# Optimization experiments

Hardware: AMD Instinct MI355X
Metric: run time of the kernel (lower is better)

The kernel has to match this reference:

```python
import jax, jax.numpy as jnp
import numpy as np

NUM_HEADS = 16


def _rope(x, c, s):
    # x: [T, H, D]; c, s: [T, D/2] -> rotate-half RoPE over full head_dim
    d2 = c.shape[-1]
    x1, x2 = x[..., :d2], x[..., d2:]
    c = c[:, None, :]
    s = s[:, None, :]
    return jnp.concatenate([x1 * c - x2 * s, x2 * c + x1 * s], axis=-1)


def setup_inputs() -> dict:
    key = jax.random.key(0)
    ks = jax.random.split(key, 4)
    B, L, dim = 8, 1024, 1024
    T = B * L
    D = dim // NUM_HEADS
    hidden_states = jax.random.normal(ks[0], (T, dim), dtype=jnp.float32)
    w_qkv = jax.random.normal(ks[1], (dim, 3 * dim), dtype=jnp.float32) * (dim ** -0.5)
    b_qkv = jnp.zeros((3 * dim,), dtype=jnp.float32)
    w_proj = jax.random.normal(ks[2], (dim, dim), dtype=jnp.float32) * (dim ** -0.5)
    b_proj = jnp.zeros((dim,), dtype=jnp.float32)
    # RoPE tables: positions restart at 0 for each packed sequence
    pos = jnp.tile(jnp.arange(L, dtype=jnp.float32), B)  # [T]
    inv_freq = 1.0 / (10000.0 ** (jnp.arange(0, D, 2, dtype=jnp.float32) / D))  # [D/2]
    freqs = pos[:, None] * inv_freq[None, :]  # [T, D/2]
    emb = jnp.concatenate([freqs, freqs], axis=-1)  # [T, D]
    cos = jnp.cos(emb)
    sin = jnp.sin(emb)
    cu_seqlens = (jnp.arange(B + 1, dtype=jnp.int32) * L)
    return {"hidden_states": hidden_states, "cos": cos, "sin": sin,
            "w_qkv": w_qkv, "b_qkv": b_qkv, "w_proj": w_proj, "b_proj": b_proj,
            "cu_seqlens": cu_seqlens}


def reference(hidden_states, cos, sin, w_qkv, b_qkv, w_proj, b_proj, cu_seqlens):
    T, dim = hidden_states.shape
    H = NUM_HEADS
    D = dim // H
    B = cu_seqlens.shape[0] - 1  # equal-length packed sequences
    L = T // B

    qkv = hidden_states @ w_qkv + b_qkv            # [T, 3*dim]
    qkv = qkv.reshape(T, 3, H, D)
    q, k, v = qkv[:, 0], qkv[:, 1], qkv[:, 2]       # [T, H, D]

    # module chunks cos/sin in half along last dim before apply_rotary_emb
    c = cos[..., : D // 2].astype(jnp.float32)
    s = sin[..., : D // 2].astype(jnp.float32)
    q = _rope(q.astype(jnp.float32), c, s).astype(hidden_states.dtype)
    k = _rope(k.astype(jnp.float32), c, s).astype(hidden_states.dtype)

    # varlen flash attention == block-diagonal attention; equal lengths -> reshape
    qb = q.reshape(B, L, H, D)
    kb = k.reshape(B, L, H, D)
    vb = v.reshape(B, L, H, D)
    scale = D ** -0.5
    scores = jnp.einsum("bqhd,bkhd->bhqk", qb, kb) * scale  # [B, H, L, L]
    probs = jax.nn.softmax(scores, axis=-1)
    out = jnp.einsum("bhqk,bkhd->bqhd", probs, vb)           # [B, L, H, D]
    out = out.reshape(T, dim)
    return out @ w_proj + b_proj
```

## Files before the change

kernel.cpp:

```cpp
#include <hip/hip_runtime.h>

typedef unsigned short ushort_t;
typedef __attribute__((ext_vector_type(8))) short short8;
typedef __attribute__((ext_vector_type(4))) float f32x4;

#define AS1 __attribute__((address_space(1)))
#define AS3 __attribute__((address_space(3)))

__device__ __forceinline__ ushort_t f2bf(float f) {
  unsigned int u = __builtin_bit_cast(unsigned int, f);
  u += 0x7fffu + ((u >> 16) & 1u);
  return (ushort_t)(u >> 16);
}

__device__ __forceinline__ unsigned int pack_bf2(float a, float b) {
  unsigned int ua = __builtin_bit_cast(unsigned int, a) + 0x8000u;
  unsigned int ub = __builtin_bit_cast(unsigned int, b) + 0x8000u;
  return (ua >> 16) | (ub & 0xffff0000u);
}

#if defined(__has_builtin)
#if __has_builtin(__builtin_amdgcn_cvt_pk_bf16_f32)
#define HAVE_CVT_PK_BF16 1
#endif
#if __has_builtin(__builtin_amdgcn_exp2f)
#define HAVE_EXP2 1
#endif
#endif

__device__ __forceinline__ unsigned int pack2(float a, float b) {
#ifdef HAVE_CVT_PK_BF16
  typedef __attribute__((ext_vector_type(2))) __bf16 bf2_t;
  bf2_t r = __builtin_amdgcn_cvt_pk_bf16_f32(a, b);
  return __builtin_bit_cast(unsigned int, r);
#else
  return pack_bf2(a, b);
#endif
}

__device__ __forceinline__ float fast_exp2(float x) {
#ifdef HAVE_EXP2
  return __builtin_amdgcn_exp2f(x);
#else
  return exp2f(x);
#endif
}

__device__ __forceinline__ void load_lds16(const ushort_t* g, ushort_t* l) {
  __builtin_amdgcn_global_load_lds((AS1 void*)g, (AS3 void*)l, 16, 0, 0);
}

#define MFMA16(a, b, c) __builtin_amdgcn_mfma_f32_16x16x32_bf16((a), (b), (c), 0, 0, 0)

__global__ __launch_bounds__(256) void k_prep(const float* __restrict__ hs,
                                              ushort_t* __restrict__ hsb,
                                              const float* __restrict__ wqkv,
                                              ushort_t* __restrict__ wqkvT,
                                              const float* __restrict__ wproj,
                                              ushort_t* __restrict__ wprojT) {
  __shared__ ushort_t t[64 * 65];
  const int bid = blockIdx.x;
  if (bid < 4096) {
    int i = bid * 256 + threadIdx.x;
    const float4* s4 = (const float4*)hs;
    float4 a = s4[(size_t)i * 2], b = s4[(size_t)i * 2 + 1];
    short8 o;
    o[0] = (short)f2bf(a.x); o[1] = (short)f2bf(a.y);
    o[2] = (short)f2bf(a.z); o[3] = (short)f2bf(a.w);
    o[4] = (short)f2bf(b.x); o[5] = (short)f2bf(b.y);
    o[6] = (short)f2bf(b.z); o[7] = (short)f2bf(b.w);
    *(short8*)(hsb + (size_t)i * 8) = o;
    return;
  }
  const float* src;
  ushort_t* dst;
  int C, bx, by;
  if (bid < 4864) { int idx = bid - 4096; src = wqkv; dst = wqkvT; C = 3072;
                    bx = idx % 48; by = idx / 48; }
  else            { int idx = bid - 4864; src = wproj; dst = wprojT; C = 1024;
                    bx = idx & 15; by = idx >> 4; }
  const int R = 1024;
  const int x0 = bx * 64, y0 = by * 64;
  const int c = threadIdx.x & 63, r0 = threadIdx.x >> 6;
#pragma unroll
  for (int i = 0; i < 16; ++i) {
    int r = r0 + i * 4;
    t[c * 65 + r] = f2bf(src[(size_t)(y0 + r) * C + x0 + c]);
  }
  __syncthreads();
#pragma unroll
  for (int i = 0; i < 16; ++i) {
    int rr = r0 + i * 4;
    dst[(size_t)(x0 + rr) * R + y0 + c] = t[rr * 65 + c];
  }
}

__global__ __launch_bounds__(512) void k_qkv_gemm_rope(
    const ushort_t* __restrict__ A, const ushort_t* __restrict__ Bt,
    const float* __restrict__ bias, const float* __restrict__ cosb,
    const float* __restrict__ sinb, ushort_t* __restrict__ Qb,
    ushort_t* __restrict__ Kb, ushort_t* __restrict__ Vp) {
  constexpr int K = 1024;
  __shared__ __align__(16) ushort_t As[256 * 64];
  __shared__ __align__(16) ushort_t Bs[128 * 64];
  const int tid = threadIdx.x, lane = tid & 63, wave = tid >> 6;
  const int quad = lane >> 4, ml = lane & 15;
  const int wm = wave & 3, wn = wave >> 2;
  const int L = blockIdx.x, xcd = L & 7, j = L >> 3;
  const int by = xcd * 4 + j / 24, bx = j % 24;
  const int m0 = by * 256, n0 = bx * 128;
  f32x4 acc[4][4] = {};

  for (int kt = 0; kt < K / 64; ++kt) {
    __syncthreads();
    {
      const int kk0 = kt * 64;
#pragma unroll
      for (int i = 0; i < 4; ++i) {
        int cch = i * 512 + tid;
        int r = cch >> 3, s = cch & 7, gs = s ^ (r & 7);
        load_lds16(A + (size_t)(m0 + r) * K + kk0 + gs * 8, As + cch * 8);
      }
#pragma unroll
      for (int i = 0; i < 2; ++i) {
        int cch = i * 512 + tid;
        int r = cch >> 3, s = cch & 7, gs = s ^ (r & 7);
        load_lds16(Bt + (size_t)(n0 + r) * K + kk0 + gs * 8, Bs + cch * 8);
      }
    }
    __syncthreads();
#pragma unroll
    for (int ks = 0; ks < 2; ++ks) {
      short8 af[4], bfr[4];
#pragma unroll
      for (int mb = 0; mb < 4; ++mb) {
        int row = wm * 64 + mb * 16 + ml;
        int gs = (ks * 4 + quad) ^ (row & 7);
        af[mb] = *(const short8*)(As + row * 64 + gs * 8);
      }
#pragma unroll
      for (int nb = 0; nb < 4; ++nb) {
        int row = wn * 64 + nb * 16 + ml;
        int gs = (ks * 4 + quad) ^ (row & 7);
        bfr[nb] = *(const short8*)(Bs + row * 64 + gs * 8);
      }
#pragma unroll
      for (int mb = 0; mb < 4; ++mb)
#pragma unroll
        for (int nb = 0; nb < 4; ++nb)
          acc[mb][nb] = MFMA16(af[mb], bfr[nb], acc[mb][nb]);
    }
  }

  const int ncol0 = n0 + wn * 64;
  const int sec = ncol0 >> 10;
  const int h = (ncol0 & 1023) >> 6;
  if (sec < 2) {
    ushort_t* dst = (sec == 0) ? Qb : Kb;
    const float qs = (sec == 0) ? 0.18033688011112042f : 1.0f;
#pragma unroll
    for (int mb = 0; mb < 4; ++mb) {
#pragma unroll
      for (int rg = 0; rg < 4; ++rg) {
        const int m = m0 + wm * 64 + mb * 16 + quad * 4 + rg;
        const int b = m >> 10, l = m & 1023;
        const size_t ob = ((size_t)(b * 16 + h) * 1024 + l) * 64;
#pragma unroll
        for (int nb = 0; nb < 2; ++nb) {
          const int d = nb * 16 + ml;
          float x1 = acc[mb][nb][rg] + bias[ncol0 + d];
          float x2 = acc[mb][nb + 2][rg] + bias[ncol0 + d + 32];
          float cv = cosb[(size_t)m * 64 + d] * qs;
          float sv = sinb[(size_t)m * 64 + d] * qs;
          dst[ob + d] = f2bf(x1 * cv - x2 * sv);
          dst[ob + d + 32] = f2bf(x2 * cv + x1 * sv);
        }
      }
    }
  } else {
    const int mrow = m0 + wm * 64;
    const int b = mrow >> 10, lB = mrow & 1023;
    ushort_t* vb = Vp + ((size_t)(b * 16 + h)) * 65536 + lB;
#pragma unroll
    for (int rg = 0; rg < 4; ++rg) {
#pragma unroll
      for (int nb = 0; nb < 4; ++nb) {
        const int d = nb * 16 + ml;
        const float bs = bias[ncol0 + d];
        uint2 w;
        w.x = pack_bf2(acc[0][nb][rg] + bs, acc[1][nb][rg] + bs);
        w.y = pack_bf2(acc[2][nb][rg] + bs, acc[3][nb][rg] + bs);
        *(uint2*)(vb + (size_t)d * 1024 + 16 * quad + 4 * rg) = w;
      }
    }
  }
}

__global__ __launch_bounds__(256, 4) void k_attn(const ushort_t* __restrict__ Qb,
                                                 const ushort_t* __restrict__ Kb,
                                                 const ushort_t* __restrict__ Vp,
                                                 ushort_t* __restrict__ Ob) {
  __shared__ __align__(16) ushort_t QP[8192];
  __shared__ __align__(16) ushort_t Ks[2][64 * 64];
  __shared__ __align__(16) ushort_t Vts[64 * 64];
  const int tid = threadIdx.x, lane = tid & 63, wave = tid >> 6;
  const int quad = lane >> 4, ml = lane & 15;
  const int bh = blockIdx.x & 127, qt = blockIdx.x >> 7;
  const int q0 = qt * 128;
  const size_t base = (size_t)bh * 65536;

#pragma unroll
  for (int i = 0; i < 4; ++i) {
    int cch = i * 256 + tid;
    int r = cch >> 3, s = cch & 7, gs = s ^ (r & 7);
    load_lds16(Qb + base + (size_t)(q0 + r) * 64 + gs * 8, QP + cch * 8);
  }
  __syncthreads();

  short8 qf[2][2];
#pragma unroll
  for (int mb = 0; mb < 2; ++mb)
#pragma unroll
    for (int ks = 0; ks < 2; ++ks) {
      int row = wave * 32 + mb * 16 + ml;
      int gs = (ks * 4 + quad) ^ (row & 7);
      qf[mb][ks] = *(const short8*)(QP + row * 64 + gs * 8);
    }

  ushort_t* Pw = QP + wave * 2048;

  const ushort_t* kg[2];
  const ushort_t* vg[2];
  ushort_t *kl[2], *vl[2];
#pragma unroll
  for (int i = 0; i < 2; ++i) {
    int cch = i * 256 + tid;
    int r = cch >> 3, gs = (cch & 7) ^ (r & 7);
    kg[i] = Kb + base + (size_t)r * 64 + gs * 8;
    kl[i] = Ks[0] + cch * 8;
    vg[i] = Vp + base + (size_t)r * 1024 + gs * 8;
    vl[i] = Vts + cch * 8;
  }
  const ushort_t* kfp[4][2];
  const ushort_t* vfp[4][2];
#pragma unroll
  for (int nb = 0; nb < 4; ++nb)
#pragma unroll
    for (int ks = 0; ks < 2; ++ks) {
      int row = nb * 16 + ml;
      int gs = (ks * 4 + quad) ^ (row & 7);
      kfp[nb][ks] = Ks[0] + row * 64 + gs * 8;
      vfp[nb][ks] = Vts + row * 64 + gs * 8;
    }
  const ushort_t* pfp[2][2];
#pragma unroll
  for (int mb = 0; mb < 2; ++mb)
#pragma unroll
    for (int ks = 0; ks < 2; ++ks) {
      int row = mb * 16 + ml;
      int gs = ((ks * 4 + quad) ^ row) & 7;
      pfp[mb][ks] = Pw + row * 64 + gs * 8;
    }
  ushort_t* pwp[2][4];
#pragma unroll
  for (int mb = 0; mb < 2; ++mb)
#pragma unroll
    for (int rg = 0; rg < 4; ++rg) {
      int row = mb * 16 + quad * 4 + rg;
      int g = ((ml >> 1) ^ row) & 7;
      pwp[mb][rg] = Pw + row * 64 + g * 8 + (ml & 1) * 4;
    }

  f32x4 Oacc[2][4] = {};
  float lsum[2][4] = {};

#pragma unroll
  for (int i = 0; i < 2; ++i) { load_lds16(kg[i], kl[i]); kg[i] += 4096; }
  __syncthreads();

#define ATTN_STEP(CUR, LAST)                                                  \
  {                                                                           \
    _Pragma("unroll") for (int i = 0; i < 2; ++i) {                           \
      load_lds16(vg[i], vl[i]);                                               \
      vg[i] += 64;                                                            \
      if (!(LAST)) {                                                          \
        load_lds16(kg[i], kl[i] + ((CUR) ^ 1) * 4096);                        \
        kg[i] += 4096;                                                        \
      }                                                                       \
    }                                                                         \
    f32x4 Sacc[2][4] = {};                                                    \
    __builtin_amdgcn_s_setprio(1);                                            \
    _Pragma("unroll") for (int nb = 0; nb < 4; ++nb)                          \
      _Pragma("unroll") for (int ks = 0; ks < 2; ++ks) {                      \
        short8 kf = *(const short8*)(kfp[nb][ks] + (CUR) * 4096);             \
        Sacc[0][nb] = MFMA16(qf[0][ks], kf, Sacc[0][nb]);                     \
        Sacc[1][nb] = MFMA16(qf[1][ks], kf, Sacc[1][nb]);                     \
      }                                                                       \
    __builtin_amdgcn_s_setprio(0);                                            \
    _Pragma("unroll") for (int mb = 0; mb < 2; ++mb) {                        \
      _Pragma("unroll") for (int rg = 0; rg < 4; ++rg) {                      \
        float p0 = fast_exp2(Sacc[mb][0][rg]);                                \
        float p1 = fast_exp2(Sacc[mb][1][rg]);                                \
        float p2 = fast_exp2(Sacc[mb][2][rg]);                                \
        float p3 = fast_exp2(Sacc[mb][3][rg]);                                \
        lsum[mb][rg] += (p0 + p1) + (p2 + p3);                                \
        uint2 w;                                                              \
        w.x = pack2(p0, p1);                                                  \
        w.y = pack2(p2, p3);                                                  \
        *(uint2*)pwp[mb][rg] = w;                                             \
      }                                                                       \
    }                                                                         \
    __syncthreads();                                                          \
    __builtin_amdgcn_s_setprio(1);                                            \
    _Pragma("unroll") for (int ks = 0; ks < 2; ++ks) {                        \
      short8 pf0 = *(const short8*)pfp[0][ks];                                \
      short8 pf1 = *(const short8*)pfp[1][ks];                                \
      _Pragma("unroll") for (int nb = 0; nb < 4; ++nb) {                      \
        short8 vf = *(const short8*)vfp[nb][ks];                              \
        Oacc[0][nb] = MFMA16(pf0, vf, Oacc[0][nb]);                           \
        Oacc[1][nb] = MFMA16(pf1, vf, Oacc[1][nb]);                           \
      }                                                                       \
    }                                                                         \
    __builtin_amdgcn_s_setprio(0);                                            \
    __syncthreads();                                                          \
  }

#pragma unroll 1
  for (int kt2 = 0; kt2 < 8; ++kt2) {
    ATTN_STEP(0, false)
    ATTN_STEP(1, kt2 == 7)
  }
#undef ATTN_STEP

  const int b = bh >> 4, h = bh & 15;
#pragma unroll
  for (int mb = 0; mb < 2; ++mb) {
#pragma unroll
    for (int rg = 0; rg < 4; ++rg) {
      float l = lsum[mb][rg];
      l += __shfl_xor(l, 1);
      l += __shfl_xor(l, 2);
      l += __shfl_xor(l, 4);
      l += __shfl_xor(l, 8);
      float inv = 1.f / l;
      int q = q0 + wave * 32 + mb * 16 + quad * 4 + rg;
      size_t ob = ((size_t)(b * 1024 + q)) * 1024 + h * 64;
#pragma unroll
      for (int nb = 0; nb < 4; ++nb)
        Ob[ob + nb * 16 + ml] = f2bf(Oacc[mb][nb][rg] * inv);
    }
  }
}

__global__ __launch_bounds__(256) void k_proj_gemm(const ushort_t* __restrict__ A,
                                                   const ushort_t* __restrict__ Bt,
                                                   const float* __restrict__ bias,
                                                   float* __restrict__ out) {
  constexpr int K = 1024;
  __shared__ __align__(16) ushort_t As[128 * 128];
  __shared__ __align__(16) ushort_t Bs[128 * 128];
  const int tid = threadIdx.x, lane = tid & 63, wave = tid >> 6;
  const int quad = lane >> 4, ml = lane & 15;
  const int wm = wave & 1, wn = wave >> 1;
  const int L = blockIdx.x, xcd = L & 7, j = L >> 3;
  const int by = xcd * 8 + (j >> 3), bx = j & 7;
  const int m0 = by * 128, n0 = bx * 128;
  f32x4 acc[4][4] = {};

  for (int kt = 0; kt < K / 128; ++kt) {
    __syncthreads();
    {
      const int kk0 = kt * 128;
#pragma unroll
      for (int i = 0; i < 8; ++i) {
        int cch = i * 256 + tid;
        int r = cch >> 4, s = cch & 15, gs = s ^ (r & 15);
        load_lds16(A + (size_t)(m0 + r) * K + kk0 + gs * 8, As + cch * 8);
        load_lds16(Bt + (size_t)(n0 + r) * K + kk0 + gs * 8, Bs + cch * 8);
      }
    }
    __syncthreads();
#pragma unroll
    for (int ks = 0; ks < 4; ++ks) {
      short8 af[4], bfr[4];
#pragma unroll
      for (int mb = 0; mb < 4; ++mb) {
        int row = wm * 64 + mb * 16 + ml;
        int gs = (ks * 4 + quad) ^ (row & 15);
        af[mb] = *(const short8*)(As + row * 128 + gs * 8);
      }
#pragma unroll
      for (int nb = 0; nb < 4; ++nb) {
        int row = wn * 64 + nb * 16 + ml;
        int gs = (ks * 4 + quad) ^ (row & 15);
        bfr[nb] = *(const short8*)(Bs + row * 128 + gs * 8);
      }
#pragma unroll
      for (int mb = 0; mb < 4; ++mb)
#pragma unroll
        for (int nb = 0; nb < 4; ++nb)
          acc[mb][nb] = MFMA16(af[mb], bfr[nb], acc[mb][nb]);
    }
  }
#pragma unroll
  for (int mb = 0; mb < 4; ++mb) {
#pragma unroll
    for (int rg = 0; rg < 4; ++rg) {
      const int m = m0 + wm * 64 + mb * 16 + quad * 4 + rg;
#pragma unroll
      for (int nb = 0; nb < 4; ++nb) {
        const int n = n0 + wn * 64 + nb * 16 + ml;
        out[(size_t)m * 1024 + n] = acc[mb][nb][rg] + bias[n];
      }
    }
  }
}

extern "C" void kernel_launch(void* const* d_in, const int* in_sizes, int n_in,
                              void* d_out, int out_size, void* d_ws, size_t ws_size,
                              hipStream_t stream) {
  const float* hs = (const float*)d_in[0];
  const float* cosb = (const float*)d_in[1];
  const float* sinb = (const float*)d_in[2];
  const float* wqkv = (const float*)d_in[3];
  const float* bqkv = (const float*)d_in[4];
  const float* wproj = (const float*)d_in[5];
  const float* bproj = (const float*)d_in[6];
  float* out = (float*)d_out;

  char* ws = (char*)d_ws;
  ushort_t* hsb = (ushort_t*)(ws);
  ushort_t* wqkvT = (ushort_t*)(ws + (16u << 20));
  ushort_t* wprojT = (ushort_t*)(ws + (22u << 20));
  ushort_t* Qb = (ushort_t*)(ws + (24u << 20));
  ushort_t* Kb = (ushort_t*)(ws + (40u << 20));
  ushort_t* Vp = (ushort_t*)(ws + (56u << 20));
  ushort_t* attnb = hsb;

  k_prep<<<5120, 256, 0, stream>>>(hs, hsb, wqkv, wqkvT, wproj, wprojT);
  k_qkv_gemm_rope<<<768, 512, 0, stream>>>(hsb, wqkvT, bqkv, cosb, sinb,
                                           Qb, Kb, Vp);
  k_attn<<<1024, 256, 0, stream>>>(Qb, Kb, Vp, attnb);
  k_proj_gemm<<<512, 256, 0, stream>>>(attnb, wprojT, bproj, out);
}
```

Baseline: 249.9 us.

## Double-buffer QKV GEMM LDS tiles and enlarge attention blocks to 256 queries

The QKV GEMM switches from single-buffered 64-wide K tiles with two barriers per step to double-buffered 32-wide K tiles, prefetching the next tile while MFMAs run, with one barrier per step. The attention kernel moves to 512-thread blocks covering 256 queries and double-buffers both K and V tiles. This halves the grid and drops one barrier per step. The changes aim to hide global-load latency and cut sync overhead, at the cost of more LDS per block and more K-loop iterations in the GEMM.

```diff
diff --git a/kernel.cpp b/kernel.cpp
--- a/kernel.cpp
+++ b/kernel.cpp
@@ -101,8 +101,8 @@
     const float* __restrict__ sinb, ushort_t* __restrict__ Qb,
     ushort_t* __restrict__ Kb, ushort_t* __restrict__ Vp) {
   constexpr int K = 1024;
-  __shared__ __align__(16) ushort_t As[256 * 64];
-  __shared__ __align__(16) ushort_t Bs[128 * 64];
+  __shared__ __align__(16) ushort_t As[2 * 8192];
+  __shared__ __align__(16) ushort_t Bs[2 * 4096];
   const int tid = threadIdx.x, lane = tid & 63, wave = tid >> 6;
   const int quad = lane >> 4, ml = lane & 15;
   const int wm = wave & 3, wn = wave >> 2;
@@ -111,46 +111,59 @@
   const int m0 = by * 256, n0 = bx * 128;
   f32x4 acc[4][4] = {};
 
-  for (int kt = 0; kt < K / 64; ++kt) {
-    __syncthreads();
-    {
-      const int kk0 = kt * 64;
-#pragma unroll
-      for (int i = 0; i < 4; ++i) {
-        int cch = i * 512 + tid;
-        int r = cch >> 3, s = cch & 7, gs = s ^ (r & 7);
-        load_lds16(A + (size_t)(m0 + r) * K + kk0 + gs * 8, As + cch * 8);
-      }
-#pragma unroll
-      for (int i = 0; i < 2; ++i) {
-        int cch = i * 512 + tid;
-        int r = cch >> 3, s = cch & 7, gs = s ^ (r & 7);
-        load_lds16(Bt + (size_t)(n0 + r) * K + kk0 + gs * 8, Bs + cch * 8);
-      }
-    }
-    __syncthreads();
-#pragma unroll
-    for (int ks = 0; ks < 2; ++ks) {
-      short8 af[4], bfr[4];
-#pragma unroll
-      for (int mb = 0; mb < 4; ++mb) {
-        int row = wm * 64 + mb * 16 + ml;
-        int gs = (ks * 4 + quad) ^ (row & 7);
-        af[mb] = *(const short8*)(As + row * 64 + gs * 8);
-      }
-#pragma unroll
-      for (int nb = 0; nb < 4; ++nb) {
-        int row = wn * 64 + nb * 16 + ml;
-        int gs = (ks * 4 + quad) ^ (row & 7);
-        bfr[nb] = *(const short8*)(Bs + row * 64 + gs * 8);
-      }
-#pragma unroll
-      for (int mb = 0; mb < 4; ++mb)
-#pragma unroll
-        for (int nb = 0; nb < 4; ++nb)
-          acc[mb][nb] = MFMA16(af[mb], bfr[nb], acc[mb][nb]);
-    }
-  }
+  const int cA0 = tid, cA1 = tid + 512, cB = tid;
+  const int rA0 = cA0 >> 2, rA1 = cA1 >> 2, rB = cB >> 2;
+  const int sA0 = (cA0 & 3) ^ ((rA0 >> 1) & 3);
+  const int sA1 = (cA1 & 3) ^ ((rA1 >> 1) & 3);
+  const int sB  = (cB & 3) ^ ((rB >> 1) & 3);
+  const ushort_t* agp0 = A + (size_t)(m0 + rA0) * K + sA0 * 8;
+  const ushort_t* agp1 = A + (size_t)(m0 + rA1) * K + sA1 * 8;
+  const ushort_t* bgp  = Bt + (size_t)(n0 + rB) * K + sB * 8;
+  ushort_t* al0 = As + cA0 * 8;
+  ushort_t* al1 = As + cA1 * 8;
+  ushort_t* bl0 = Bs + cB * 8;
+
+  int afo[4], bfo[4];
+#pragma unroll
+  for (int mb = 0; mb < 4; ++mb) {
+    int row = wm * 64 + mb * 16 + ml;
+    afo[mb] = row * 32 + ((quad ^ ((row >> 1) & 3)) & 3) * 8;
+  }
+#pragma unroll
+  for (int nb = 0; nb < 4; ++nb) {
+    int row = wn * 64 + nb * 16 + ml;
+    bfo[nb] = row * 32 + ((quad ^ ((row >> 1) & 3)) & 3) * 8;
+  }
+
+  load_lds16(agp0, al0); agp0 += 32;
+  load_lds16(agp1, al1); agp1 += 32;
+  load_lds16(bgp, bl0);  bgp += 32;
+  __syncthreads();
+
+#define QKV_STEP(CUR, LAST)                                                   \
+  {                                                                           \
+    if (!(LAST)) {                                                            \
+      load_lds16(agp0, al0 + ((CUR) ^ 1) * 8192); agp0 += 32;                 \
+      load_lds16(agp1, al1 + ((CUR) ^ 1) * 8192); agp1 += 32;                 \
+      load_lds16(bgp,  bl0 + ((CUR) ^ 1) * 4096); bgp  += 32;                 \
+    }                                                                         \
+    short8 af[4], bfr[4];                                                     \
+    _Pragma("unroll") for (int mb = 0; mb < 4; ++mb)                          \
+        af[mb] = *(const short8*)(As + (CUR) * 8192 + afo[mb]);               \
+    _Pragma("unroll") for (int nb = 0; nb < 4; ++nb)                          \
+        bfr[nb] = *(const short8*)(Bs + (CUR) * 4096 + bfo[nb]);              \
+    _Pragma("unroll") for (int mb = 0; mb < 4; ++mb)                          \
+      _Pragma("unroll") for (int nb = 0; nb < 4; ++nb)                        \
+          acc[mb][nb] = MFMA16(af[mb], bfr[nb], acc[mb][nb]);                 \
+    __syncthreads();                                                          \
+  }
+
+#pragma unroll 1
+  for (int t2 = 0; t2 < 16; ++t2) {
+    QKV_STEP(0, false)
+    QKV_STEP(1, t2 == 15)
+  }
+#undef QKV_STEP
 
   const int ncol0 = n0 + wn * 64;
   const int sec = ncol0 >> 10;
@@ -196,25 +209,39 @@
   }
 }
 
-__global__ __launch_bounds__(256, 4) void k_attn(const ushort_t* __restrict__ Qb,
+__global__ __launch_bounds__(512, 4) void k_attn(const ushort_t* __restrict__ Qb,
                                                  const ushort_t* __restrict__ Kb,
                                                  const ushort_t* __restrict__ Vp,
                                                  ushort_t* __restrict__ Ob) {
-  __shared__ __align__(16) ushort_t QP[8192];
-  __shared__ __align__(16) ushort_t Ks[2][64 * 64];
-  __shared__ __align__(16) ushort_t Vts[64 * 64];
+  __shared__ __align__(16) ushort_t QP[16384];
+  __shared__ __align__(16) ushort_t Ks[2][4096];
+  __shared__ __align__(16) ushort_t Vts[2][4096];
   const int tid = threadIdx.x, lane = tid & 63, wave = tid >> 6;
   const int quad = lane >> 4, ml = lane & 15;
   const int bh = blockIdx.x & 127, qt = blockIdx.x >> 7;
-  const int q0 = qt * 128;
+  const int q0 = qt * 256;
   const size_t base = (size_t)bh * 65536;
 
 #pragma unroll
   for (int i = 0; i < 4; ++i) {
-    int cch = i * 256 + tid;
+    int cch = i * 512 + tid;
     int r = cch >> 3, s = cch & 7, gs = s ^ (r & 7);
     load_lds16(Qb + base + (size_t)(q0 + r) * 64 + gs * 8, QP + cch * 8);
   }
+
+  const ushort_t* kg;
+  const ushort_t* vg;
+  ushort_t *kl, *vl;
+  {
+    int cch = tid;
+    int r = cch >> 3, gs = (cch & 7) ^ (r & 7);
+    kg = Kb + base + (size_t)r * 64 + gs * 8;
+    kl = Ks[0] + cch * 8;
+    vg = Vp + base + (size_t)r * 1024 + gs * 8;
+    vl = Vts[0] + cch * 8;
+  }
+  load_lds16(kg, kl); kg += 4096;
+  load_lds16(vg, vl); vg += 64;
   __syncthreads();
 
   short8 qf[2][2];
@@ -226,21 +253,10 @@
       int gs = (ks * 4 + quad) ^ (row & 7);
       qf[mb][ks] = *(const short8*)(QP + row * 64 + gs * 8);
     }
+  __syncthreads();
 
   ushort_t* Pw = QP + wave * 2048;
 
-  const ushort_t* kg[2];
-  const ushort_t* vg[2];
-  ushort_t *kl[2], *vl[2];
-#pragma unroll
-  for (int i = 0; i < 2; ++i) {
-    int cch = i * 256 + tid;
-    int r = cch >> 3, gs = (cch & 7) ^ (r & 7);
-    kg[i] = Kb + base + (size_t)r * 64 + gs * 8;
-    kl[i] = Ks[0] + cch * 8;
-    vg[i] = Vp + base + (size_t)r * 1024 + gs * 8;
-    vl[i] = Vts + cch * 8;
-  }
   const ushort_t* kfp[4][2];
   const ushort_t* vfp[4][2];
 #pragma unroll
@@ -250,7 +266,7 @@
       int row = nb * 16 + ml;
       int gs = (ks * 4 + quad) ^ (row & 7);
       kfp[nb][ks] = Ks[0] + row * 64 + gs * 8;
-      vfp[nb][ks] = Vts + row * 64 + gs * 8;
+      vfp[nb][ks] = Vts[0] + row * 64 + gs * 8;
     }
   const ushort_t* pfp[2][2];
 #pragma unroll
@@ -274,19 +290,11 @@
   f32x4 Oacc[2][4] = {};
   float lsum[2][4] = {};
 
-#pragma unroll
-  for (int i = 0; i < 2; ++i) { load_lds16(kg[i], kl[i]); kg[i] += 4096; }
-  __syncthreads();
-
 #define ATTN_STEP(CUR, LAST)                                                  \
   {                                                                           \
-    _Pragma("unroll") for (int i = 0; i < 2; ++i) {                           \
-      load_lds16(vg[i], vl[i]);                                               \
-      vg[i] += 64;                                                            \
-      if (!(LAST)) {                                                          \
-        load_lds16(kg[i], kl[i] + ((CUR) ^ 1) * 4096);                        \
-        kg[i] += 4096;                                                        \
-      }                                                                       \
+    if (!(LAST)) {                                                            \
+      load_lds16(kg, kl + ((CUR) ^ 1) * 4096); kg += 4096;                    \
+      load_lds16(vg, vl + ((CUR) ^ 1) * 4096); vg += 64;                      \
     }                                                                         \
     f32x4 Sacc[2][4] = {};                                                    \
     __builtin_amdgcn_s_setprio(1);                                            \
@@ -310,13 +318,12 @@
         *(uint2*)pwp[mb][rg] = w;                                             \
       }                                                                       \
     }                                                                         \
-    __syncthreads();                                                          \
     __builtin_amdgcn_s_setprio(1);                                            \
     _Pragma("unroll") for (int ks = 0; ks < 2; ++ks) {                        \
       short8 pf0 = *(const short8*)pfp[0][ks];                                \
       short8 pf1 = *(const short8*)pfp[1][ks];                                \
       _Pragma("unroll") for (int nb = 0; nb < 4; ++nb) {                      \
-        short8 vf = *(const short8*)vfp[nb][ks];                              \
+        short8 vf = *(const short8*)(vfp[nb][ks] + (CUR) * 4096);             \
         Oacc[0][nb] = MFMA16(pf0, vf, Oacc[0][nb]);                           \
         Oacc[1][nb] = MFMA16(pf1, vf, Oacc[1][nb]);                           \
       }                                                                       \
@@ -440,6 +447,6 @@
   k_prep<<<5120, 256, 0, stream>>>(hs, hsb, wqkv, wqkvT, wproj, wprojT);
   k_qkv_gemm_rope<<<768, 512, 0, stream>>>(hsb, wqkvT, bqkv, cosb, sinb,
                                            Qb, Kb, Vp);
-  k_attn<<<1024, 256, 0, stream>>>(Qb, Kb, Vp, attnb);
+  k_attn<<<512, 512, 0, stream>>>(Qb, Kb, Vp, attnb);
   k_proj_gemm<<<512, 256, 0, stream>>>(attnb, wprojT, bproj, out);
 }
```

New measurement: 252.2 us. Within noise of the previous version (+0.9%).

## Shrink QKV GEMM tiles and enlarge attention blocks with double-buffered V

Applied to the files above, without the earlier changes.

The QKV GEMM drops from 256x128 tiles with 512 threads to 128x128 tiles with 256 threads, doubling the grid. The attention kernel moves to 512-thread blocks covering 256 query rows. V is now double-buffered alongside K and prefetched one step ahead, which removes the barrier between the P writes and the PV MFMAs. This aims to overlap K/V loads with compute and cut synchronisation, at the cost of more LDS per block. Each K/V tile is also shared across twice as many waves.

```diff
diff --git a/kernel.cpp b/kernel.cpp
--- a/kernel.cpp
+++ b/kernel.cpp
@@ -95,20 +95,20 @@
   }
 }
 
-__global__ __launch_bounds__(512) void k_qkv_gemm_rope(
+__global__ __launch_bounds__(256) void k_qkv_gemm_rope(
     const ushort_t* __restrict__ A, const ushort_t* __restrict__ Bt,
     const float* __restrict__ bias, const float* __restrict__ cosb,
     const float* __restrict__ sinb, ushort_t* __restrict__ Qb,
     ushort_t* __restrict__ Kb, ushort_t* __restrict__ Vp) {
   constexpr int K = 1024;
-  __shared__ __align__(16) ushort_t As[256 * 64];
+  __shared__ __align__(16) ushort_t As[128 * 64];
   __shared__ __align__(16) ushort_t Bs[128 * 64];
   const int tid = threadIdx.x, lane = tid & 63, wave = tid >> 6;
   const int quad = lane >> 4, ml = lane & 15;
-  const int wm = wave & 3, wn = wave >> 2;
+  const int wm = wave & 1, wn = wave >> 1;
   const int L = blockIdx.x, xcd = L & 7, j = L >> 3;
-  const int by = xcd * 4 + j / 24, bx = j % 24;
-  const int m0 = by * 256, n0 = bx * 128;
+  const int by = xcd * 8 + j / 24, bx = j % 24;
+  const int m0 = by * 128, n0 = bx * 128;
   f32x4 acc[4][4] = {};
 
   for (int kt = 0; kt < K / 64; ++kt) {
@@ -117,13 +117,13 @@
       const int kk0 = kt * 64;
 #pragma unroll
       for (int i = 0; i < 4; ++i) {
-        int cch = i * 512 + tid;
+        int cch = i * 256 + tid;
         int r = cch >> 3, s = cch & 7, gs = s ^ (r & 7);
         load_lds16(A + (size_t)(m0 + r) * K + kk0 + gs * 8, As + cch * 8);
       }
 #pragma unroll
-      for (int i = 0; i < 2; ++i) {
-        int cch = i * 512 + tid;
+      for (int i = 0; i < 4; ++i) {
+        int cch = i * 256 + tid;
         int r = cch >> 3, s = cch & 7, gs = s ^ (r & 7);
         load_lds16(Bt + (size_t)(n0 + r) * K + kk0 + gs * 8, Bs + cch * 8);
       }
@@ -196,25 +196,39 @@
   }
 }
 
-__global__ __launch_bounds__(256, 4) void k_attn(const ushort_t* __restrict__ Qb,
+__global__ __launch_bounds__(512, 4) void k_attn(const ushort_t* __restrict__ Qb,
                                                  const ushort_t* __restrict__ Kb,
                                                  const ushort_t* __restrict__ Vp,
                                                  ushort_t* __restrict__ Ob) {
-  __shared__ __align__(16) ushort_t QP[8192];
-  __shared__ __align__(16) ushort_t Ks[2][64 * 64];
-  __shared__ __align__(16) ushort_t Vts[64 * 64];
+  __shared__ __align__(16) ushort_t QP[16384];
+  __shared__ __align__(16) ushort_t Ks[2][4096];
+  __shared__ __align__(16) ushort_t Vts[2][4096];
   const int tid = threadIdx.x, lane = tid & 63, wave = tid >> 6;
   const int quad = lane >> 4, ml = lane & 15;
   const int bh = blockIdx.x & 127, qt = blockIdx.x >> 7;
-  const int q0 = qt * 128;
+  const int q0 = qt * 256;
   const size_t base = (size_t)bh * 65536;
 
 #pragma unroll
   for (int i = 0; i < 4; ++i) {
-    int cch = i * 256 + tid;
+    int cch = i * 512 + tid;
     int r = cch >> 3, s = cch & 7, gs = s ^ (r & 7);
     load_lds16(Qb + base + (size_t)(q0 + r) * 64 + gs * 8, QP + cch * 8);
   }
+
+  const ushort_t* kg;
+  const ushort_t* vg;
+  ushort_t *kl, *vl;
+  {
+    int cch = tid;
+    int r = cch >> 3, gs = (cch & 7) ^ (r & 7);
+    kg = Kb + base + (size_t)r * 64 + gs * 8;
+    kl = Ks[0] + cch * 8;
+    vg = Vp + base + (size_t)r * 1024 + gs * 8;
+    vl = Vts[0] + cch * 8;
+  }
+  load_lds16(kg, kl); kg += 4096;
+  load_lds16(vg, vl); vg += 64;
   __syncthreads();
 
   short8 qf[2][2];
@@ -226,21 +240,10 @@
       int gs = (ks * 4 + quad) ^ (row & 7);
       qf[mb][ks] = *(const short8*)(QP + row * 64 + gs * 8);
     }
+  __syncthreads();
 
   ushort_t* Pw = QP + wave * 2048;
 
-  const ushort_t* kg[2];
-  const ushort_t* vg[2];
-  ushort_t *kl[2], *vl[2];
-#pragma unroll
-  for (int i = 0; i < 2; ++i) {
-    int cch = i * 256 + tid;
-    int r = cch >> 3, gs = (cch & 7) ^ (r & 7);
-    kg[i] = Kb + base + (size_t)r * 64 + gs * 8;
-    kl[i] = Ks[0] + cch * 8;
-    vg[i] = Vp + base + (size_t)r * 1024 + gs * 8;
-    vl[i] = Vts + cch * 8;
-  }
   const ushort_t* kfp[4][2];
   const ushort_t* vfp[4][2];
 #pragma unroll
@@ -250,7 +253,7 @@
       int row = nb * 16 + ml;
       int gs = (ks * 4 + quad) ^ (row & 7);
       kfp[nb][ks] = Ks[0] + row * 64 + gs * 8;
-      vfp[nb][ks] = Vts + row * 64 + gs * 8;
+      vfp[nb][ks] = Vts[0] + row * 64 + gs * 8;
     }
   const ushort_t* pfp[2][2];
 #pragma unroll
@@ -274,19 +277,11 @@
   f32x4 Oacc[2][4] = {};
   float lsum[2][4] = {};
 
-#pragma unroll
-  for (int i = 0; i < 2; ++i) { load_lds16(kg[i], kl[i]); kg[i] += 4096; }
-  __syncthreads();
-
 #define ATTN_STEP(CUR, LAST)                                                  \
   {                                                                           \
-    _Pragma("unroll") for (int i = 0; i < 2; ++i) {                           \
-      load_lds16(vg[i], vl[i]);                                               \
-      vg[i] += 64;                                                            \
-      if (!(LAST)) {                                                          \
-        load_lds16(kg[i], kl[i] + ((CUR) ^ 1) * 4096);                        \
-        kg[i] += 4096;                                                        \
-      }                                                                       \
+    if (!(LAST)) {                                                            \
+      load_lds16(kg, kl + ((CUR) ^ 1) * 4096); kg += 4096;                    \
+      load_lds16(vg, vl + ((CUR) ^ 1) * 4096); vg += 64;                      \
     }                                                                         \
     f32x4 Sacc[2][4] = {};                                                    \
     __builtin_amdgcn_s_setprio(1);                                            \
@@ -310,13 +305,12 @@
         *(uint2*)pwp[mb][rg] = w;                                             \
       }                                                                       \
     }                                                                         \
-    __syncthreads();                                                          \
     __builtin_amdgcn_s_setprio(1);                                            \
     _Pragma("unroll") for (int ks = 0; ks < 2; ++ks) {                        \
       short8 pf0 = *(const short8*)pfp[0][ks];                                \
       short8 pf1 = *(const short8*)pfp[1][ks];                                \
       _Pragma("unroll") for (int nb = 0; nb < 4; ++nb) {                      \
-        short8 vf = *(const short8*)vfp[nb][ks];                              \
+        short8 vf = *(const short8*)(vfp[nb][ks] + (CUR) * 4096);             \
         Oacc[0][nb] = MFMA16(pf0, vf, Oacc[0][nb]);                           \
         Oacc[1][nb] = MFMA16(pf1, vf, Oacc[1][nb]);                           \
       }                                                                       \
@@ -438,8 +432,8 @@
   ushort_t* attnb = hsb;
 
   k_prep<<<5120, 256, 0, stream>>>(hs, hsb, wqkv, wqkvT, wproj, wprojT);
-  k_qkv_gemm_rope<<<768, 512, 0, stream>>>(hsb, wqkvT, bqkv, cosb, sinb,
-                                           Qb, Kb, Vp);
-  k_attn<<<1024, 256, 0, stream>>>(Qb, Kb, Vp, attnb);
+  k_qkv_gemm_rope<<<1536, 256, 0, stream>>>(hsb, wqkvT, bqkv, cosb, sinb,
+                                            Qb, Kb, Vp);
+  k_attn<<<512, 512, 0, stream>>>(Qb, Kb, Vp, attnb);
   k_proj_gemm<<<512, 256, 0, stream>>>(attnb, wprojT, bproj, out);
 }
```

Result: slower. 261.8 us (+4.8%).
